# Performance work log

Measured on AMD Instinct MI355X. Metric: run time of the kernel, lower is better.

The kernel has to match this reference:

```python
import jax, jax.numpy as jnp
from jax import lax
import numpy as np

DEPTH = 6
DIM = 512            # embed_dim
DI = 768             # d_inner = int(1.5 * 512)
B = 64
IMG = 224
P = 16               # patch size == stride
HW = 14              # patches per side
NP = HW * HW         # 196


def _ln(x, w, b, eps=1e-5):
    m = jnp.mean(x, axis=-1, keepdims=True)
    v = jnp.var(x, axis=-1, keepdims=True)
    return (x - m) / jnp.sqrt(v + eps) * w + b


def _mamba(x, in_w, out_w, cw, cb, dw, db, A, D):
    # x: (N, L, DIM); in_w: (2*DI, DIM); out_w: (DIM, DI); cw: (DI, 3)
    xz = jnp.einsum('nlc,dc->nld', x, in_w)          # (N, L, 2*DI)
    xi, z = jnp.split(xz, 2, axis=-1)
    # depthwise conv1d, kernel=3, padding=1
    xp = jnp.pad(xi, ((0, 0), (1, 1), (0, 0)))
    xc = xp[:, :-2] * cw[:, 0] + xp[:, 1:-1] * cw[:, 1] + xp[:, 2:] * cw[:, 2] + cb
    xc = jax.nn.silu(xc)
    dt = jax.nn.softplus(jnp.einsum('nld,ed->nle', xc, dw) + db)
    Ae = jnp.exp(A * dt)                              # A < 0, dt > 0 -> stable
    y = jnp.cumsum(xc * dt * Ae, axis=1) * Ae + xc * D
    y = y * jax.nn.silu(z)
    return jnp.einsum('nld,cd->nlc', y, out_w)


def _forward(x, patch_w, patch_b, cls_token, pos_embed,
             blk_norm_w, blk_norm_b,
             mh_in_w, mh_out_w, mh_conv_w, mh_conv_b, mh_dt_w, mh_dt_b, mh_A, mh_D,
             mv_in_w, mv_out_w, mv_conv_w, mv_conv_b, mv_dt_w, mv_dt_b, mv_A, mv_D,
             fus_w, fus_b, ss_norm_w, ss_norm_b, fn_w, fn_b):
    Bsz = x.shape[0]
    # patch embed: Conv2d(3, DIM, k=16, s=16)
    feat = lax.conv_general_dilated(x, patch_w, window_strides=(P, P), padding='VALID',
                                    dimension_numbers=('NCHW', 'OIHW', 'NCHW'))
    feat = feat + patch_b[None, :, None, None]
    feat = feat.reshape(Bsz, DIM, NP).transpose(0, 2, 1)  # (B, 196, DIM)
    tok = jnp.concatenate([jnp.broadcast_to(cls_token, (Bsz, 1, DIM)), feat], axis=1)
    tok = tok + pos_embed                                  # (B, 197, DIM)
    for i in range(DEPTH):
        cls = tok[:, :1]
        pt = tok[:, 1:]
        pn = _ln(pt, blk_norm_w[i], blk_norm_b[i])
        p2 = pn.reshape(Bsz, HW, HW, DIM)
        # horizontal scan: rows as sequences
        yh = _mamba(p2.reshape(Bsz * HW, HW, DIM),
                    mh_in_w[i], mh_out_w[i], mh_conv_w[i], mh_conv_b[i],
                    mh_dt_w[i], mh_dt_b[i], mh_A[i], mh_D[i]).reshape(Bsz, HW, HW, DIM)
        # vertical scan: columns as sequences
        xv = p2.transpose(0, 2, 1, 3).reshape(Bsz * HW, HW, DIM)
        yv = _mamba(xv,
                    mv_in_w[i], mv_out_w[i], mv_conv_w[i], mv_conv_b[i],
                    mv_dt_w[i], mv_dt_b[i], mv_A[i], mv_D[i])
        yv = yv.reshape(Bsz, HW, HW, DIM).transpose(0, 2, 1, 3)
        yc = jnp.concatenate([yh, yv], axis=-1)            # (B, H, W, 2*DIM)
        yf = jnp.einsum('bhwk,ck->bhwc', yc, fus_w[i]) + fus_b[i]
        p_out = _ln(yf + p2, ss_norm_w[i], ss_norm_b[i]).reshape(Bsz, NP, DIM)
        cls_out = cls + _ln(cls, blk_norm_w[i], blk_norm_b[i])
        tok = jnp.concatenate([cls_out, p_out], axis=1)
    return _ln(tok, fn_w, fn_b)


def setup_inputs() -> dict:
    key = jax.random.key(0)
    ks = jax.random.split(key, 32)
    s = 0.02
    d = {}
    d['x'] = jax.random.normal(ks[0], (B, 3, IMG, IMG), jnp.float32)
    d['patch_w'] = jax.random.normal(ks[1], (DIM, 3, P, P), jnp.float32) * s
    d['patch_b'] = jnp.zeros((DIM,), jnp.float32)
    d['cls_token'] = jax.random.normal(ks[2], (1, 1, DIM), jnp.float32) * s
    d['pos_embed'] = jax.random.normal(ks[3], (1, NP + 1, DIM), jnp.float32) * s
    d['blk_norm_w'] = jnp.ones((DEPTH, DIM), jnp.float32)
    d['blk_norm_b'] = jnp.zeros((DEPTH, DIM), jnp.float32)
    for pfx, base in (('mh', 4), ('mv', 12)):
        d[pfx + '_in_w'] = jax.random.normal(ks[base + 0], (DEPTH, 2 * DI, DIM), jnp.float32) * s
        d[pfx + '_out_w'] = jax.random.normal(ks[base + 1], (DEPTH, DIM, DI), jnp.float32) * s
        d[pfx + '_conv_w'] = jax.random.normal(ks[base + 2], (DEPTH, DI, 3), jnp.float32) * 0.2
        d[pfx + '_conv_b'] = jnp.zeros((DEPTH, DI), jnp.float32)
        d[pfx + '_dt_w'] = jax.random.normal(ks[base + 3], (DEPTH, DI, DI), jnp.float32) * s
        d[pfx + '_dt_b'] = jnp.zeros((DEPTH, DI), jnp.float32)
        d[pfx + '_A'] = -jax.random.uniform(ks[base + 4], (DEPTH, DI), jnp.float32) * 0.1
        d[pfx + '_D'] = jnp.ones((DEPTH, DI), jnp.float32)
    d['fus_w'] = jax.random.normal(ks[20], (DEPTH, DIM, 2 * DIM), jnp.float32) * s
    d['fus_b'] = jnp.zeros((DEPTH, DIM), jnp.float32)
    d['ss_norm_w'] = jnp.ones((DEPTH, DIM), jnp.float32)
    d['ss_norm_b'] = jnp.zeros((DEPTH, DIM), jnp.float32)
    d['fn_w'] = jnp.ones((DIM,), jnp.float32)
    d['fn_b'] = jnp.zeros((DIM,), jnp.float32)
    return d


def reference(x, patch_w, patch_b, cls_token, pos_embed,
              blk_norm_w, blk_norm_b,
              mh_in_w, mh_out_w, mh_conv_w, mh_conv_b, mh_dt_w, mh_dt_b, mh_A, mh_D,
              mv_in_w, mv_out_w, mv_conv_w, mv_conv_b, mv_dt_w, mv_dt_b, mv_A, mv_D,
              fus_w, fus_b, ss_norm_w, ss_norm_b, fn_w, fn_b):
    return _forward(x, patch_w, patch_b, cls_token, pos_embed,
                    blk_norm_w, blk_norm_b,
                    mh_in_w, mh_out_w, mh_conv_w, mh_conv_b, mh_dt_w, mh_dt_b, mh_A, mh_D,
                    mv_in_w, mv_out_w, mv_conv_w, mv_conv_b, mv_dt_w, mv_dt_b, mv_A, mv_D,
                    fus_w, fus_b, ss_norm_w, ss_norm_b, fn_w, fn_b)
```

## Files before the change

kernel.cpp:

```cpp
#include <hip/hip_runtime.h>
#include <cstdint>


using u16 = unsigned short;
typedef __attribute__((ext_vector_type(8))) short   bfrag;
typedef __attribute__((ext_vector_type(4))) float   ffrag;
typedef __attribute__((ext_vector_type(8))) u16     u16x8;
typedef __attribute__((ext_vector_type(4))) u16     u16x4;

__device__ __forceinline__ float b2f(u16 u) {
  union { float f; uint32_t i; } c; c.i = ((uint32_t)u) << 16; return c.f;
}
__device__ __forceinline__ u16 f2b(float f) {
  union { float f; uint32_t i; } c; c.f = f;
  uint32_t r = c.i + 0x7FFFu + ((c.i >> 16) & 1u);
  return (u16)(r >> 16);
}

#define LOG2E 1.44269504f
#define LN2   0.69314718f
__device__ __forceinline__ float fexp(float x) {
  return __builtin_amdgcn_exp2f(x * LOG2E);
}
__device__ __forceinline__ float fsigmoid(float x) {
  return __builtin_amdgcn_rcpf(1.f + __builtin_amdgcn_exp2f(-x * LOG2E));
}
__device__ __forceinline__ float fsilu(float x) { return x * fsigmoid(x); }
__device__ __forceinline__ float fsoftplus(float x) {
  float e = __builtin_amdgcn_exp2f(-fabsf(x) * LOG2E);
  return fmaxf(x, 0.f) + LN2 * __builtin_amdgcn_logf(1.f + e);
}

__device__ __forceinline__ void gl_lds16(const u16* g, u16* l) {
  __builtin_amdgcn_global_load_lds(
      (const __attribute__((address_space(1))) void*)g,
      (__attribute__((address_space(3))) void*)l,
      16, 0, 0);
}

__global__ __launch_bounds__(256, 2)
void gemm_dual(const u16* __restrict__ A, const u16* __restrict__ W1,
               const u16* __restrict__ W2, u16* __restrict__ C,
               int K, int lda, int ldc, int nsplit, int acol2, int ccol2)
{
  __shared__ u16 As[128 * 64];
  __shared__ u16 Bs[128 * 64];

  const int total = gridDim.x * gridDim.y;
  const int flat  = blockIdx.y * gridDim.x + blockIdx.x;
  const int chunk = total >> 3;
  const int f2    = (flat & 7) * chunk + (flat >> 3);
  const int bx    = f2 % gridDim.x;
  const int by    = f2 / gridDim.x;

  const bool second = bx >= nsplit;
  const u16* W     = second ? W2 : W1;
  const int n0l    = (bx - (second ? nsplit : 0)) * 128;
  const int acol   = second ? acol2 : 0;
  const int ccol0  = n0l + (second ? ccol2 : 0);
  const int m0     = by * 128;

  const int tid  = threadIdx.x;
  const int lane = tid & 63;
  const int wv   = tid >> 6;
  const int wm   = wv >> 1;
  const int wn   = wv & 1;

  const int lr   = lane >> 3;
  const int lc   = lane & 7;
  const int kcol = (lc ^ lr) << 3;

  const size_t abase = (size_t)(m0 + wv * 32 + lr) * lda + acol + kcol;
  const size_t wbase = (size_t)(n0l + wv * 32 + lr) * K + kcol;

  const ffrag fz = {0.f, 0.f, 0.f, 0.f};
  ffrag acc[4][4];
#pragma unroll
  for (int i = 0; i < 4; ++i)
#pragma unroll
    for (int j = 0; j < 4; ++j) acc[i][j] = fz;

  const int fr = lane & 15;
  const int fq = lane >> 4;

  for (int kb = 0; kb < K; kb += 64) {
#pragma unroll
    for (int i = 0; i < 4; ++i)
      gl_lds16(A + abase + (size_t)(i * 8) * lda + kb, &As[(wv * 4 + i) * 512]);
#pragma unroll
    for (int i = 0; i < 4; ++i)
      gl_lds16(W + wbase + (size_t)(i * 8) * K + kb, &Bs[(wv * 4 + i) * 512]);
    __syncthreads();

#pragma unroll
    for (int ks = 0; ks < 2; ++ks) {
      bfrag af[4], bfr[4];
#pragma unroll
      for (int t = 0; t < 4; ++t) {
        int r  = wm * 64 + t * 16 + fr;
        int ca = ((ks * 4 + fq) ^ (r & 7)) << 3;
        af[t]  = *(const bfrag*)&As[r * 64 + ca];
        int n  = wn * 64 + t * 16 + fr;
        int cb = ((ks * 4 + fq) ^ (n & 7)) << 3;
        bfr[t] = *(const bfrag*)&Bs[n * 64 + cb];
      }
#pragma unroll
      for (int i = 0; i < 4; ++i)
#pragma unroll
        for (int j = 0; j < 4; ++j)
          acc[i][j] = __builtin_amdgcn_mfma_f32_16x16x32_bf16(
              af[i], bfr[j], acc[i][j], 0, 0, 0);
    }
    __syncthreads();
  }

#pragma unroll
  for (int i = 0; i < 4; ++i)
#pragma unroll
    for (int j = 0; j < 4; ++j)
#pragma unroll
      for (int rg = 0; rg < 4; ++rg) {
        int row = m0 + wm * 64 + i * 16 + fq * 4 + rg;
        int col = ccol0 + wn * 64 + j * 16 + fr;
        C[(size_t)row * ldc + col] = f2b(acc[i][j][rg]);
      }
}

__global__ __launch_bounds__(256, 2)
void gemm_wprep(const u16* __restrict__ WB, const u16* __restrict__ OT,
                u16* __restrict__ WF)
{
  __shared__ u16 As[128 * 64];
  __shared__ u16 Bs[128 * 64];

  const int z = blockIdx.z, L = z >> 1, path = z & 1;
  const u16* A = WB + (size_t)L * 4063232 + 3538944;
  const u16* W = OT + (size_t)z * 393216;
  u16* C = WF + (size_t)L * 786432;

  const int m0 = blockIdx.y * 128, n0l = blockIdx.x * 128;
  const int acol = path * 512, ccol = path * 768;

  const int tid  = threadIdx.x;
  const int lane = tid & 63;
  const int wv   = tid >> 6;
  const int wm   = wv >> 1;
  const int wn   = wv & 1;
  const int lr   = lane >> 3;
  const int lc   = lane & 7;
  const int kcol = (lc ^ lr) << 3;

  const size_t abase = (size_t)(m0 + wv * 32 + lr) * 1024 + acol + kcol;
  const size_t wbase = (size_t)(n0l + wv * 32 + lr) * 512 + kcol;

  const ffrag fz = {0.f, 0.f, 0.f, 0.f};
  ffrag acc[4][4];
#pragma unroll
  for (int i = 0; i < 4; ++i)
#pragma unroll
    for (int j = 0; j < 4; ++j) acc[i][j] = fz;

  const int fr = lane & 15;
  const int fq = lane >> 4;

  for (int kb = 0; kb < 512; kb += 64) {
#pragma unroll
    for (int i = 0; i < 4; ++i)
      gl_lds16(A + abase + (size_t)(i * 8) * 1024 + kb, &As[(wv * 4 + i) * 512]);
#pragma unroll
    for (int i = 0; i < 4; ++i)
      gl_lds16(W + wbase + (size_t)(i * 8) * 512 + kb, &Bs[(wv * 4 + i) * 512]);
    __syncthreads();

#pragma unroll
    for (int ks = 0; ks < 2; ++ks) {
      bfrag af[4], bfr[4];
#pragma unroll
      for (int t = 0; t < 4; ++t) {
        int r  = wm * 64 + t * 16 + fr;
        int ca = ((ks * 4 + fq) ^ (r & 7)) << 3;
        af[t]  = *(const bfrag*)&As[r * 64 + ca];
        int n  = wn * 64 + t * 16 + fr;
        int cb = ((ks * 4 + fq) ^ (n & 7)) << 3;
        bfr[t] = *(const bfrag*)&Bs[n * 64 + cb];
      }
#pragma unroll
      for (int i = 0; i < 4; ++i)
#pragma unroll
        for (int j = 0; j < 4; ++j)
          acc[i][j] = __builtin_amdgcn_mfma_f32_16x16x32_bf16(
              af[i], bfr[j], acc[i][j], 0, 0, 0);
    }
    __syncthreads();
  }

#pragma unroll
  for (int i = 0; i < 4; ++i)
#pragma unroll
    for (int j = 0; j < 4; ++j)
#pragma unroll
      for (int rg = 0; rg < 4; ++rg) {
        int row = m0 + wm * 64 + i * 16 + fq * 4 + rg;
        int col = ccol + n0l + wn * 64 + j * 16 + fr;
        C[(size_t)row * 1536 + col] = f2b(acc[i][j][rg]);
      }
}

__global__ __launch_bounds__(256)
void k_transp(const float* __restrict__ mho, const float* __restrict__ mvo,
              u16* __restrict__ OT)
{
  __shared__ float ld[32][33];
  const int z = blockIdx.z, L = z >> 1, path = z & 1;
  const float* src = (path ? mvo : mho) + (size_t)L * 393216;
  u16* dst = OT + (size_t)z * 393216;
  const int tx = threadIdx.x & 31, ty = threadIdx.x >> 5;
  const int dx = blockIdx.x * 32, cy = blockIdx.y * 32;
#pragma unroll
  for (int i = 0; i < 4; ++i)
    ld[ty + 8 * i][tx] = src[(size_t)(cy + ty + 8 * i) * 768 + dx + tx];
  __syncthreads();
#pragma unroll
  for (int i = 0; i < 4; ++i)
    dst[(size_t)(dx + ty + 8 * i) * 512 + cy + tx] = f2b(ld[tx][ty + 8 * i]);
}

__global__ __launch_bounds__(256)
void k_cvt_all(const float* __restrict__ mhi, const float* __restrict__ mhd,
               const float* __restrict__ mvi, const float* __restrict__ mvd,
               const float* __restrict__ fus, u16* __restrict__ dst)
{
  size_t e = ((size_t)blockIdx.x * 256 + threadIdx.x) * 8;
  int L = (int)(e / 3276800);
  int r = (int)(e - (size_t)L * 3276800);
  const float* s; int off; int dsto;
  if      (r <  786432) { s = mhi + (size_t)L * 786432; off = r;           dsto = r; }
  else if (r < 1376256) { s = mhd + (size_t)L * 589824; off = r -  786432; dsto = r; }
  else if (r < 2162688) { s = mvi + (size_t)L * 786432; off = r - 1376256; dsto = r + 393216; }
  else if (r < 2752512) { s = mvd + (size_t)L * 589824; off = r - 2162688; dsto = r + 393216; }
  else                  { s = fus + (size_t)L * 524288; off = r - 2752512; dsto = r + 786432; }
  float4 a = *(const float4*)(s + off);
  float4 b = *(const float4*)(s + off + 4);
  u16x8 o;
  o[0] = f2b(a.x); o[1] = f2b(a.y); o[2] = f2b(a.z); o[3] = f2b(a.w);
  o[4] = f2b(b.x); o[5] = f2b(b.y); o[6] = f2b(b.z); o[7] = f2b(b.w);
  *(u16x8*)(dst + (size_t)L * 4063232 + dsto) = o;
}

__global__ __launch_bounds__(256)
void k_cvt1(const float* __restrict__ s, u16* __restrict__ dst)
{
  int e = (blockIdx.x * 256 + threadIdx.x) * 8;
  float4 a = *(const float4*)(s + e);
  float4 b = *(const float4*)(s + e + 4);
  u16x8 o;
  o[0] = f2b(a.x); o[1] = f2b(a.y); o[2] = f2b(a.z); o[3] = f2b(a.w);
  o[4] = f2b(b.x); o[5] = f2b(b.y); o[6] = f2b(b.z); o[7] = f2b(b.w);
  *(u16x8*)(dst + e) = o;
}

__global__ __launch_bounds__(256) void k_im2col(const float* __restrict__ x,
                                                u16* __restrict__ im)
{
  int idx = blockIdx.x * 256 + threadIdx.x;
  int r = idx % 96, p = idx / 96;
  int b = p / 196, q = p - b * 196;
  int ph = q / 14, pw = q - ph * 14;
  int k = r * 8;
  int c = k >> 8, k2 = k & 255;
  int i = k2 >> 4, j = k2 & 15;
  const float* src = x + (((size_t)(b * 3 + c) * 224 + ph * 16 + i) * 224
                          + pw * 16 + j);
  float4 a = *(const float4*)src;
  float4 d = *(const float4*)(src + 4);
  u16x8 o;
  o[0] = f2b(a.x); o[1] = f2b(a.y); o[2] = f2b(a.z); o[3] = f2b(a.w);
  o[4] = f2b(d.x); o[5] = f2b(d.y); o[6] = f2b(d.z); o[7] = f2b(d.w);
  *(u16x8*)(im + (size_t)p * 768 + k) = o;
}

__global__ __launch_bounds__(256)
void k_addbias_ln(u16* __restrict__ TOK, const float* __restrict__ pb,
                  const float* __restrict__ pos, const float* __restrict__ w,
                  const float* __restrict__ b)
{
  int row  = blockIdx.x * 4 + (threadIdx.x >> 6);
  int lane = threadIdx.x & 63;
  int base = lane * 8;
  int tpos = 1 + (row % 196);
  u16* p = TOK + (size_t)row * 512 + base;
  u16x8 t = *(u16x8*)p;
  const float* pv = pos + (size_t)tpos * 512 + base;
  float v[8]; float s = 0.f, qq = 0.f;
#pragma unroll
  for (int i = 0; i < 8; ++i) {
    v[i] = b2f(t[i]) + pb[base + i] + pv[i];
    s += v[i]; qq += v[i] * v[i];
  }
#pragma unroll
  for (int o = 32; o; o >>= 1) { s += __shfl_xor(s, o, 64); qq += __shfl_xor(qq, o, 64); }
  float mean = s * (1.f / 512.f);
  float rstd = rsqrtf(qq * (1.f / 512.f) - mean * mean + 1e-5f);
  u16x8 ov;
#pragma unroll
  for (int i = 0; i < 8; ++i)
    ov[i] = f2b((v[i] - mean) * rstd * w[base + i] + b[base + i]);
  *(u16x8*)p = ov;
}

__global__ __launch_bounds__(256) void k_ln_fuse(const u16* __restrict__ YF,
                                                 u16* __restrict__ TOK,
                                                 const float* __restrict__ fb,
                                                 const float* __restrict__ w,
                                                 const float* __restrict__ b)
{
  int row  = blockIdx.x * 4 + (threadIdx.x >> 6);
  int lane = threadIdx.x & 63;
  int base = lane * 8;
  const u16* yf = YF + (size_t)row * 512 + base;
  u16* tp = TOK + (size_t)row * 512 + base;
  u16x8 yv = *(const u16x8*)yf;
  u16x8 tv = *(u16x8*)tp;
  float v[8]; float s = 0.f, qq = 0.f;
#pragma unroll
  for (int i = 0; i < 8; ++i) {
    v[i] = b2f(yv[i]) + fb[base + i] + b2f(tv[i]);
    s += v[i]; qq += v[i] * v[i];
  }
#pragma unroll
  for (int o = 32; o; o >>= 1) { s += __shfl_xor(s, o, 64); qq += __shfl_xor(qq, o, 64); }
  float mean = s * (1.f / 512.f);
  float rstd = rsqrtf(qq * (1.f / 512.f) - mean * mean + 1e-5f);
  u16x8 ov;
#pragma unroll
  for (int i = 0; i < 8; ++i)
    ov[i] = f2b((v[i] - mean) * rstd * w[base + i] + b[base + i]);
  *(u16x8*)tp = ov;
}

__global__ __launch_bounds__(256)
void k_ln_fuse2(const u16* __restrict__ YF, u16* __restrict__ TOK,
                const float* __restrict__ fb, const float* __restrict__ w1,
                const float* __restrict__ b1, const float* __restrict__ w2,
                const float* __restrict__ b2)
{
  int row  = blockIdx.x * 4 + (threadIdx.x >> 6);
  int lane = threadIdx.x & 63;
  int base = lane * 8;
  const u16* yf = YF + (size_t)row * 512 + base;
  u16* tp = TOK + (size_t)row * 512 + base;
  u16x8 yv = *(const u16x8*)yf;
  u16x8 tv = *(u16x8*)tp;
  float v[8]; float s = 0.f, qq = 0.f;
#pragma unroll
  for (int i = 0; i < 8; ++i) {
    v[i] = b2f(yv[i]) + fb[base + i] + b2f(tv[i]);
    s += v[i]; qq += v[i] * v[i];
  }
#pragma unroll
  for (int o = 32; o; o >>= 1) { s += __shfl_xor(s, o, 64); qq += __shfl_xor(qq, o, 64); }
  float mean = s * (1.f / 512.f);
  float rstd = rsqrtf(qq * (1.f / 512.f) - mean * mean + 1e-5f);
  float s2 = 0.f, q2 = 0.f;
#pragma unroll
  for (int i = 0; i < 8; ++i) {
    v[i] = (v[i] - mean) * rstd * w1[base + i] + b1[base + i];
    s2 += v[i]; q2 += v[i] * v[i];
  }
#pragma unroll
  for (int o = 32; o; o >>= 1) { s2 += __shfl_xor(s2, o, 64); q2 += __shfl_xor(q2, o, 64); }
  float m2 = s2 * (1.f / 512.f);
  float r2 = rsqrtf(q2 * (1.f / 512.f) - m2 * m2 + 1e-5f);
  u16x8 ov;
#pragma unroll
  for (int i = 0; i < 8; ++i)
    ov[i] = f2b((v[i] - m2) * r2 * w2[base + i] + b2[base + i]);
  *(u16x8*)tp = ov;
}

__global__ __launch_bounds__(256)
void k_conv_hv(const u16* __restrict__ XZ,
               const float* __restrict__ cwh, const float* __restrict__ cbh,
               const float* __restrict__ cwv, const float* __restrict__ cbv,
               u16* __restrict__ XC)
{
  int idx = blockIdx.x * 256 + threadIdx.x;
  int half = idx >= 172032;
  int t = idx - (half ? 172032 : 0);
  int dp = t % 192, sq = t / 192;
  int d0 = dp * 4;
  int rowbase, rowstride;
  if (!half) { rowbase = sq * 14; rowstride = 1; }
  else       { int b = sq / 14, wq = sq - b * 14; rowbase = b * 196 + wq; rowstride = 14; }
  const float* cw = half ? cwv : cwh;
  const float* cb = half ? cbv : cbh;
  int xio = half ? 1536 : 0, xco = half ? 768 : 0;
  float w0[4], w1[4], w2[4], bc[4];
#pragma unroll
  for (int i = 0; i < 4; ++i) {
    w0[i] = cw[(d0 + i) * 3 + 0];
    w1[i] = cw[(d0 + i) * 3 + 1];
    w2[i] = cw[(d0 + i) * 3 + 2];
    bc[i] = cb[d0 + i];
  }
  u16x4 cu = *(const u16x4*)&XZ[(size_t)rowbase * 3072 + xio + d0];
  float p[4] = {0.f, 0.f, 0.f, 0.f}, c[4], n[4];
#pragma unroll
  for (int i = 0; i < 4; ++i) c[i] = b2f(cu[i]);
#pragma unroll
  for (int l = 0; l < 14; ++l) {
    int row = rowbase + l * rowstride;
    if (l < 13) {
      u16x4 nu = *(const u16x4*)&XZ[(size_t)(row + rowstride) * 3072 + xio + d0];
#pragma unroll
      for (int i = 0; i < 4; ++i) n[i] = b2f(nu[i]);
    } else {
#pragma unroll
      for (int i = 0; i < 4; ++i) n[i] = 0.f;
    }
    u16x4 ov;
#pragma unroll
    for (int i = 0; i < 4; ++i)
      ov[i] = f2b(fsilu(p[i] * w0[i] + c[i] * w1[i] + n[i] * w2[i] + bc[i]));
    *(u16x4*)&XC[(size_t)row * 1536 + xco + d0] = ov;
#pragma unroll
    for (int i = 0; i < 4; ++i) { p[i] = c[i]; c[i] = n[i]; }
  }
}

__global__ __launch_bounds__(256)
void k_scan_hv(const u16* __restrict__ XZ, u16* __restrict__ XC,
               const float* __restrict__ dtbh, const float* __restrict__ Ah,
               const float* __restrict__ Dh,
               const float* __restrict__ dtbv, const float* __restrict__ Av,
               const float* __restrict__ Dv)
{
  int idx = blockIdx.x * 256 + threadIdx.x;
  int half = idx >= 172032;
  int t = idx - (half ? 172032 : 0);
  int dp = t % 192, sq = t / 192;
  int d0 = dp * 4;
  int rowbase, rowstride;
  if (!half) { rowbase = sq * 14; rowstride = 1; }
  else       { int b = sq / 14, wq = sq - b * 14; rowbase = b * 196 + wq; rowstride = 14; }
  int xio = half ? 1536 : 0, xco = half ? 768 : 0;
  const float* dtb = half ? dtbv : dtbh;
  const float* Ap  = half ? Av : Ah;
  const float* Dp  = half ? Dv : Dh;
  float db[4], Aa[4], Da[4], r[4];
#pragma unroll
  for (int i = 0; i < 4; ++i) {
    db[i] = dtb[d0 + i]; Aa[i] = Ap[d0 + i]; Da[i] = Dp[d0 + i]; r[i] = 0.f;
  }
#pragma unroll
  for (int l = 0; l < 14; ++l) {
    int row = rowbase + l * rowstride;
    size_t zb  = (size_t)row * 3072 + xio;
    size_t cbo = (size_t)row * 1536 + xco;
    u16x4 xcu = *(const u16x4*)&XC[cbo + d0];
    u16x4 dtu = *(const u16x4*)&XZ[zb + d0];
    u16x4 zu  = *(const u16x4*)&XZ[zb + 768 + d0];
    u16x4 ov;
#pragma unroll
    for (int i = 0; i < 4; ++i) {
      float xc = b2f(xcu[i]);
      float dt = fsoftplus(b2f(dtu[i]) + db[i]);
      float ae = fexp(Aa[i] * dt);
      r[i] += xc * dt * ae;
      float z = b2f(zu[i]);
      float y = (r[i] * ae + xc * Da[i]) * (z * fsigmoid(z));
      ov[i] = f2b(y);
    }
    *(u16x4*)&XC[cbo + d0] = ov;
  }
}

__global__ void k_cls(const float* __restrict__ cls_tok,
                      const float* __restrict__ pos,
                      const float* __restrict__ bw, const float* __restrict__ bb,
                      float* __restrict__ CLS)
{
  __shared__ float rs[8], rq[8], stat[2];
  int n = threadIdx.x;
  float v = cls_tok[n] + pos[n];
  for (int l = 0; l < 6; ++l) {
    float s = v, q = v * v;
#pragma unroll
    for (int o = 32; o; o >>= 1) { s += __shfl_xor(s, o, 64); q += __shfl_xor(q, o, 64); }
    if ((n & 63) == 0) { rs[n >> 6] = s; rq[n >> 6] = q; }
    __syncthreads();
    if (n == 0) {
      float S = 0.f, Q = 0.f;
      for (int i = 0; i < 8; ++i) { S += rs[i]; Q += rq[i]; }
      float m = S * (1.f / 512.f);
      stat[0] = m; stat[1] = rsqrtf(Q * (1.f / 512.f) - m * m + 1e-5f);
    }
    __syncthreads();
    float u = (v - stat[0]) * stat[1] * bw[l * 512 + n] + bb[l * 512 + n];
    v = v + u;
    __syncthreads();
  }
  CLS[n] = v;
}

__global__ __launch_bounds__(256) void k_final(const u16* __restrict__ TOK,
                                               const float* __restrict__ CLS,
                                               const float* __restrict__ w,
                                               const float* __restrict__ b,
                                               float* __restrict__ out)
{
  int row  = blockIdx.x * 4 + (threadIdx.x >> 6);
  int lane = threadIdx.x & 63;
  int bi = row / 197;
  int t  = row - bi * 197;
  int base = lane * 8;
  float v[8]; float s = 0.f, qq = 0.f;
  if (t == 0) {
#pragma unroll
    for (int i = 0; i < 8; ++i) v[i] = CLS[base + i];
  } else {
    const u16* src = TOK + ((size_t)bi * 196 + (t - 1)) * 512 + base;
    u16x8 tv = *(const u16x8*)src;
#pragma unroll
    for (int i = 0; i < 8; ++i) v[i] = b2f(tv[i]);
  }
#pragma unroll
  for (int i = 0; i < 8; ++i) { s += v[i]; qq += v[i] * v[i]; }
#pragma unroll
  for (int o = 32; o; o >>= 1) { s += __shfl_xor(s, o, 64); qq += __shfl_xor(qq, o, 64); }
  float mean = s * (1.f / 512.f);
  float rstd = rsqrtf(qq * (1.f / 512.f) - mean * mean + 1e-5f);
  float* op = out + (size_t)row * 512 + base;
#pragma unroll
  for (int i = 0; i < 8; ++i)
    op[i] = (v[i] - mean) * rstd * w[base + i] + b[base + i];
}

extern "C" void kernel_launch(void* const* d_in, const int* in_sizes, int n_in,
                              void* d_out, int out_size, void* d_ws, size_t ws_size,
                              hipStream_t stream)
{
  const float* x        = (const float*)d_in[0];
  const float* patch_w  = (const float*)d_in[1];
  const float* patch_b  = (const float*)d_in[2];
  const float* cls_tok  = (const float*)d_in[3];
  const float* pos      = (const float*)d_in[4];
  const float* blk_w    = (const float*)d_in[5];
  const float* blk_b    = (const float*)d_in[6];
  const float* mh_in_w  = (const float*)d_in[7];
  const float* mh_out_w = (const float*)d_in[8];
  const float* mh_cw    = (const float*)d_in[9];
  const float* mh_cb    = (const float*)d_in[10];
  const float* mh_dtw   = (const float*)d_in[11];
  const float* mh_dtb   = (const float*)d_in[12];
  const float* mh_A     = (const float*)d_in[13];
  const float* mh_D     = (const float*)d_in[14];
  const float* mv_in_w  = (const float*)d_in[15];
  const float* mv_out_w = (const float*)d_in[16];
  const float* mv_cw    = (const float*)d_in[17];
  const float* mv_cb    = (const float*)d_in[18];
  const float* mv_dtw   = (const float*)d_in[19];
  const float* mv_dtb   = (const float*)d_in[20];
  const float* mv_A     = (const float*)d_in[21];
  const float* mv_D     = (const float*)d_in[22];
  const float* fus_w    = (const float*)d_in[23];
  const float* fus_b    = (const float*)d_in[24];
  const float* ss_w     = (const float*)d_in[25];
  const float* ss_b     = (const float*)d_in[26];
  const float* fn_w     = (const float*)d_in[27];
  const float* fn_b     = (const float*)d_in[28];

  char* ws = (char*)d_ws;
  u16*   TOK  = (u16*)  (ws);
  u16*   XZHV = (u16*)  (ws +  12845056);
  u16*   XCHV = (u16*)  (ws +  89915392);
  u16*   WB   = (u16*)  (ws + 128450560);
  u16*   WP   = (u16*)  (ws + 177209344);
  u16*   OT   = (u16*)  (ws + 178782208);
  u16*   WF   = (u16*)  (ws + 188219392);
  float* CLS  = (float*)(ws + 197656576);
  u16*   IM   = XCHV;
  u16*   YF   = XZHV;

  const size_t LS = 4063232;
  const size_t oMHI = 0, oMHD = 786432, oMVI = 1769472, oMVD = 2555904;

  k_cvt_all<<<9600, 256, 0, stream>>>(mh_in_w, mh_dtw,
                                      mv_in_w, mv_dtw, fus_w, WB);
  k_transp<<<dim3(24, 16, 12), 256, 0, stream>>>(mh_out_w, mv_out_w, OT);
  gemm_wprep<<<dim3(6, 4, 12), 256, 0, stream>>>(WB, OT, WF);
  k_cvt1<<<192, 256, 0, stream>>>(patch_w, WP);
  k_im2col<<<4704, 256, 0, stream>>>(x, IM);
  gemm_dual<<<dim3(4, 98), 256, 0, stream>>>(IM, WP, WP, TOK,
                                             768, 768, 512, 4, 0, 0);
  k_addbias_ln<<<3136, 256, 0, stream>>>(TOK, patch_b, pos, blk_w, blk_b);
  k_cls<<<1, 512, 0, stream>>>(cls_tok, pos, blk_w, blk_b, CLS);

  for (int L = 0; L < 6; ++L) {
    const u16* wl = WB + (size_t)L * LS;

    gemm_dual<<<dim3(24, 98), 256, 0, stream>>>(
        TOK, wl + oMHI, wl + oMVI, XZHV, 512, 512, 3072, 12, 0, 1536);
    k_conv_hv<<<1344, 256, 0, stream>>>(XZHV, mh_cw + L * 2304, mh_cb + L * 768,
                                        mv_cw + L * 2304, mv_cb + L * 768, XCHV);
    gemm_dual<<<dim3(12, 98), 256, 0, stream>>>(
        XCHV, wl + oMHD, wl + oMVD, XZHV, 768, 1536, 3072, 6, 768, 1536);
    k_scan_hv<<<1344, 256, 0, stream>>>(XZHV, XCHV,
                                        mh_dtb + L * 768, mh_A + L * 768, mh_D + L * 768,
                                        mv_dtb + L * 768, mv_A + L * 768, mv_D + L * 768);
    gemm_dual<<<dim3(4, 98), 256, 0, stream>>>(
        XCHV, WF + (size_t)L * 786432, WF + (size_t)L * 786432, YF,
        1536, 1536, 512, 4, 0, 0);
    if (L < 5) {
      k_ln_fuse2<<<3136, 256, 0, stream>>>(YF, TOK, fus_b + L * 512,
                                           ss_w + L * 512, ss_b + L * 512,
                                           blk_w + (L + 1) * 512, blk_b + (L + 1) * 512);
    } else {
      k_ln_fuse<<<3136, 256, 0, stream>>>(YF, TOK, fus_b + L * 512,
                                          ss_w + L * 512, ss_b + L * 512);
    }
  }

  k_final<<<3152, 256, 0, stream>>>(TOK, CLS, fn_w, fn_b, (float*)d_out);
  (void)in_sizes; (void)n_in; (void)out_size; (void)ws_size;
}
```

Before: 1.266 ms.

## Double-buffer GEMM LDS tiles and widen conv/scan kernels to 8 channels

The bf16 GEMM now uses two LDS buffers and prefetches the next K tile with global_load_lds while MFMAs run on the current one, aiming to hide global-load latency behind compute. The depthwise conv and scan kernels process 8 channels per thread with 16-byte vector loads and stores, halving the grid. Doubling LDS per block to 64 KB may limit occupancy. Wider per-thread work raises register use and leaves fewer threads to hide latency.

```diff
diff --git a/kernel.cpp b/kernel.cpp
--- a/kernel.cpp
+++ b/kernel.cpp
@@ -43,8 +43,8 @@
                const u16* __restrict__ W2, u16* __restrict__ C,
                int K, int lda, int ldc, int nsplit, int acol2, int ccol2)
 {
-  __shared__ u16 As[128 * 64];
-  __shared__ u16 Bs[128 * 64];
+  __shared__ u16 As[2][128 * 64];
+  __shared__ u16 Bs[2][128 * 64];
 
   const int total = gridDim.x * gridDim.y;
   const int flat  = blockIdx.y * gridDim.x + blockIdx.x;
@@ -83,26 +83,34 @@
   const int fr = lane & 15;
   const int fq = lane >> 4;
 
-  for (int kb = 0; kb < K; kb += 64) {
+  auto stage = [&](int kb, int buf) {
 #pragma unroll
     for (int i = 0; i < 4; ++i)
-      gl_lds16(A + abase + (size_t)(i * 8) * lda + kb, &As[(wv * 4 + i) * 512]);
+      gl_lds16(A + abase + (size_t)(i * 8) * lda + kb, &As[buf][(wv * 4 + i) * 512]);
 #pragma unroll
     for (int i = 0; i < 4; ++i)
-      gl_lds16(W + wbase + (size_t)(i * 8) * K + kb, &Bs[(wv * 4 + i) * 512]);
-    __syncthreads();
+      gl_lds16(W + wbase + (size_t)(i * 8) * K + kb, &Bs[buf][(wv * 4 + i) * 512]);
+  };
+
+  const int nk = K >> 6;
+  stage(0, 0);
+  __syncthreads();
+
+  for (int t = 0; t < nk; ++t) {
+    const int cur = t & 1;
+    if (t + 1 < nk) stage((t + 1) * 64, cur ^ 1);
 
 #pragma unroll
     for (int ks = 0; ks < 2; ++ks) {
       bfrag af[4], bfr[4];
 #pragma unroll
-      for (int t = 0; t < 4; ++t) {
-        int r  = wm * 64 + t * 16 + fr;
+      for (int t4 = 0; t4 < 4; ++t4) {
+        int r  = wm * 64 + t4 * 16 + fr;
         int ca = ((ks * 4 + fq) ^ (r & 7)) << 3;
-        af[t]  = *(const bfrag*)&As[r * 64 + ca];
-        int n  = wn * 64 + t * 16 + fr;
+        af[t4]  = *(const bfrag*)&As[cur][r * 64 + ca];
+        int n  = wn * 64 + t4 * 16 + fr;
         int cb = ((ks * 4 + fq) ^ (n & 7)) << 3;
-        bfr[t] = *(const bfrag*)&Bs[n * 64 + cb];
+        bfr[t4] = *(const bfrag*)&Bs[cur][n * 64 + cb];
       }
 #pragma unroll
       for (int i = 0; i < 4; ++i)
@@ -385,46 +393,46 @@
                u16* __restrict__ XC)
 {
   int idx = blockIdx.x * 256 + threadIdx.x;
-  int half = idx >= 172032;
-  int t = idx - (half ? 172032 : 0);
-  int dp = t % 192, sq = t / 192;
-  int d0 = dp * 4;
+  int half = idx >= 86016;
+  int t = idx - (half ? 86016 : 0);
+  int dp = t % 96, sq = t / 96;
+  int d0 = dp * 8;
   int rowbase, rowstride;
   if (!half) { rowbase = sq * 14; rowstride = 1; }
   else       { int b = sq / 14, wq = sq - b * 14; rowbase = b * 196 + wq; rowstride = 14; }
   const float* cw = half ? cwv : cwh;
   const float* cb = half ? cbv : cbh;
   int xio = half ? 1536 : 0, xco = half ? 768 : 0;
-  float w0[4], w1[4], w2[4], bc[4];
-#pragma unroll
-  for (int i = 0; i < 4; ++i) {
+  float w0[8], w1[8], w2[8], bc[8];
+#pragma unroll
+  for (int i = 0; i < 8; ++i) {
     w0[i] = cw[(d0 + i) * 3 + 0];
     w1[i] = cw[(d0 + i) * 3 + 1];
     w2[i] = cw[(d0 + i) * 3 + 2];
     bc[i] = cb[d0 + i];
   }
-  u16x4 cu = *(const u16x4*)&XZ[(size_t)rowbase * 3072 + xio + d0];
-  float p[4] = {0.f, 0.f, 0.f, 0.f}, c[4], n[4];
-#pragma unroll
-  for (int i = 0; i < 4; ++i) c[i] = b2f(cu[i]);
+  u16x8 cu = *(const u16x8*)&XZ[(size_t)rowbase * 3072 + xio + d0];
+  float p[8], c[8], n[8];
+#pragma unroll
+  for (int i = 0; i < 8; ++i) { p[i] = 0.f; c[i] = b2f(cu[i]); }
 #pragma unroll
   for (int l = 0; l < 14; ++l) {
     int row = rowbase + l * rowstride;
     if (l < 13) {
-      u16x4 nu = *(const u16x4*)&XZ[(size_t)(row + rowstride) * 3072 + xio + d0];
-#pragma unroll
-      for (int i = 0; i < 4; ++i) n[i] = b2f(nu[i]);
+      u16x8 nu = *(const u16x8*)&XZ[(size_t)(row + rowstride) * 3072 + xio + d0];
+#pragma unroll
+      for (int i = 0; i < 8; ++i) n[i] = b2f(nu[i]);
     } else {
 #pragma unroll
-      for (int i = 0; i < 4; ++i) n[i] = 0.f;
+      for (int i = 0; i < 8; ++i) n[i] = 0.f;
     }
-    u16x4 ov;
-#pragma unroll
-    for (int i = 0; i < 4; ++i)
+    u16x8 ov;
+#pragma unroll
+    for (int i = 0; i < 8; ++i)
       ov[i] = f2b(fsilu(p[i] * w0[i] + c[i] * w1[i] + n[i] * w2[i] + bc[i]));
-    *(u16x4*)&XC[(size_t)row * 1536 + xco + d0] = ov;
-#pragma unroll
-    for (int i = 0; i < 4; ++i) { p[i] = c[i]; c[i] = n[i]; }
+    *(u16x8*)&XC[(size_t)row * 1536 + xco + d0] = ov;
+#pragma unroll
+    for (int i = 0; i < 8; ++i) { p[i] = c[i]; c[i] = n[i]; }
   }
 }
 
@@ -436,10 +444,10 @@
                const float* __restrict__ Dv)
 {
   int idx = blockIdx.x * 256 + threadIdx.x;
-  int half = idx >= 172032;
-  int t = idx - (half ? 172032 : 0);
-  int dp = t % 192, sq = t / 192;
-  int d0 = dp * 4;
+  int half = idx >= 86016;
+  int t = idx - (half ? 86016 : 0);
+  int dp = t % 96, sq = t / 96;
+  int d0 = dp * 8;
   int rowbase, rowstride;
   if (!half) { rowbase = sq * 14; rowstride = 1; }
   else       { int b = sq / 14, wq = sq - b * 14; rowbase = b * 196 + wq; rowstride = 14; }
@@ -447,9 +455,9 @@
   const float* dtb = half ? dtbv : dtbh;
   const float* Ap  = half ? Av : Ah;
   const float* Dp  = half ? Dv : Dh;
-  float db[4], Aa[4], Da[4], r[4];
-#pragma unroll
-  for (int i = 0; i < 4; ++i) {
+  float db[8], Aa[8], Da[8], r[8];
+#pragma unroll
+  for (int i = 0; i < 8; ++i) {
     db[i] = dtb[d0 + i]; Aa[i] = Ap[d0 + i]; Da[i] = Dp[d0 + i]; r[i] = 0.f;
   }
 #pragma unroll
@@ -457,12 +465,12 @@
     int row = rowbase + l * rowstride;
     size_t zb  = (size_t)row * 3072 + xio;
     size_t cbo = (size_t)row * 1536 + xco;
-    u16x4 xcu = *(const u16x4*)&XC[cbo + d0];
-    u16x4 dtu = *(const u16x4*)&XZ[zb + d0];
-    u16x4 zu  = *(const u16x4*)&XZ[zb + 768 + d0];
-    u16x4 ov;
-#pragma unroll
-    for (int i = 0; i < 4; ++i) {
+    u16x8 xcu = *(const u16x8*)&XC[cbo + d0];
+    u16x8 dtu = *(const u16x8*)&XZ[zb + d0];
+    u16x8 zu  = *(const u16x8*)&XZ[zb + 768 + d0];
+    u16x8 ov;
+#pragma unroll
+    for (int i = 0; i < 8; ++i) {
       float xc = b2f(xcu[i]);
       float dt = fsoftplus(b2f(dtu[i]) + db[i]);
       float ae = fexp(Aa[i] * dt);
@@ -471,7 +479,7 @@
       float y = (r[i] * ae + xc * Da[i]) * (z * fsigmoid(z));
       ov[i] = f2b(y);
     }
-    *(u16x4*)&XC[cbo + d0] = ov;
+    *(u16x8*)&XC[cbo + d0] = ov;
   }
 }
 
@@ -601,13 +609,13 @@
 
     gemm_dual<<<dim3(24, 98), 256, 0, stream>>>(
         TOK, wl + oMHI, wl + oMVI, XZHV, 512, 512, 3072, 12, 0, 1536);
-    k_conv_hv<<<1344, 256, 0, stream>>>(XZHV, mh_cw + L * 2304, mh_cb + L * 768,
-                                        mv_cw + L * 2304, mv_cb + L * 768, XCHV);
+    k_conv_hv<<<672, 256, 0, stream>>>(XZHV, mh_cw + L * 2304, mh_cb + L * 768,
+                                       mv_cw + L * 2304, mv_cb + L * 768, XCHV);
     gemm_dual<<<dim3(12, 98), 256, 0, stream>>>(
         XCHV, wl + oMHD, wl + oMVD, XZHV, 768, 1536, 3072, 6, 768, 1536);
-    k_scan_hv<<<1344, 256, 0, stream>>>(XZHV, XCHV,
-                                        mh_dtb + L * 768, mh_A + L * 768, mh_D + L * 768,
-                                        mv_dtb + L * 768, mv_A + L * 768, mv_D + L * 768);
+    k_scan_hv<<<672, 256, 0, stream>>>(XZHV, XCHV,
+                                       mh_dtb + L * 768, mh_A + L * 768, mh_D + L * 768,
+                                       mv_dtb + L * 768, mv_A + L * 768, mv_D + L * 768);
     gemm_dual<<<dim3(4, 98), 256, 0, stream>>>(
         XCHV, WF + (size_t)L * 786432, WF + (size_t)L * 786432, YF,
         1536, 1536, 512, 4, 0, 0);
```

New measurement: 1.311 ms. 3.5% more time.
